# Kernel tuning notes

Hardware: AMD Instinct MI355X
Metric: run time of the kernel (lower is better)

The kernel has to match this reference:

```python
import jax, jax.numpy as jnp
import numpy as np

N_HEADS = 16
R = 256.0


def setup_inputs() -> dict:
    key = jax.random.key(0)
    ks = jax.random.split(key, 8)
    B, T, D, H = 4, 1024, 1024, N_HEADS
    s = 1.0 / np.sqrt(D)
    return {
        "x": jax.random.normal(ks[0], (B, T, D), jnp.float32),
        "Wq": jax.random.normal(ks[1], (D, D), jnp.float32) * s,
        "Wk": jax.random.normal(ks[2], (D, D), jnp.float32) * s,
        "Wv": jax.random.normal(ks[3], (D, D), jnp.float32) * s,
        "Wo": jax.random.normal(ks[4], (D, D), jnp.float32) * s,
        "bo": jnp.zeros((D,), jnp.float32),
        "Wspan": jax.random.normal(ks[5], (H, D), jnp.float32) * s,
        "bspan": jnp.zeros((H,), jnp.float32),
    }


def reference(x, Wq, Wk, Wv, Wo, bo, Wspan, bspan):
    B, T, D = x.shape
    H = N_HEADS
    dh = D // H
    scale = jnp.sqrt(jnp.float32(dh))

    # projections -> (B, H, T, dh)
    def proj(W):
        return jnp.einsum('btd,ed->bte', x, W).reshape(B, T, H, dh).transpose(0, 2, 1, 3)
    Q, K, V = proj(Wq), proj(Wk), proj(Wv)

    # learned span per head: z = T * sigmoid(span_net(mean_t x))  -> (B, H)
    z = T * jax.nn.sigmoid(jnp.einsum('bd,hd->bh', x.mean(axis=1), Wspan) + bspan)

    idx = jnp.arange(T, dtype=jnp.float32)
    dist = idx[None, :] - idx[:, None]          # dist[i,j] = j - i
    causal = dist >= 0                           # matches torch code's mask
    dist_c = jnp.maximum(dist, 0.0)

    scores = jnp.einsum('bhtd,bhsd->bhts', Q, K) / scale
    scores = jnp.where(causal[None, None], scores, -jnp.inf)
    attn = jax.nn.softmax(scores, axis=-1)

    # soft span mask chi_z(h) = clamp((R + z - dist)/R, 0, 1)  (Eq 7)
    span_mask = jnp.clip((R + z[:, :, None, None] - dist_c[None, None]) / R, 0.0, 1.0)
    attn = attn * span_mask
    attn = attn / (attn.sum(axis=-1, keepdims=True) + 1e-8)
    # dropout p=0.0 (eval) -> identity

    out = jnp.einsum('bhts,bhsd->bhtd', attn, V)
    out = out.transpose(0, 2, 1, 3).reshape(B, T, D)
    return jnp.einsum('btd,ed->bte', out, Wo) + bo
```

## Files before the change

kernel.cpp:

```cpp
#include <hip/hip_runtime.h>

#define T_SEQ 1024
#define D_MODEL 1024
#define NH 16
#define DH 64
#define R_SPAN 256.0f

typedef unsigned short ushort_t;
typedef __attribute__((ext_vector_type(8))) short bf16x8;
typedef __attribute__((ext_vector_type(4))) float f32x4;

__device__ __forceinline__ ushort_t f2bf(float f){
  union { float f; unsigned u; } v; v.f = f;
  unsigned r = v.u + 0x7fffu + ((v.u >> 16) & 1u);
  return (ushort_t)(r >> 16);
}

__device__ __forceinline__ ushort_t f2bf_fast(float f){
  union { float f; unsigned u; } v; v.f = f;
  return (ushort_t)((v.u + 0x8000u) >> 16);
}

__device__ __forceinline__ float fast_exp2(float x){
#if __has_builtin(__builtin_amdgcn_exp2f)
  return __builtin_amdgcn_exp2f(x);
#else
  return __expf(x * 0.69314718056f);
#endif
}

__device__ __forceinline__ void barrier_lds_only(){
  __builtin_amdgcn_s_waitcnt(0xC07F);
  __builtin_amdgcn_s_barrier();
}

typedef __attribute__((address_space(1))) void GV;
typedef __attribute__((address_space(3))) void LV;
__device__ __forceinline__ void gld16(const void* g, void* l){
  __builtin_amdgcn_global_load_lds((GV*)g, (LV*)l, 16, 0, 0);
}

__global__ void conv_w(const float* s1, const float* s2, const float* s3, const float* s4,
                       ushort_t* __restrict__ w_bf){
  const int chunk = blockIdx.y;
  const float* ws_[4] = {s1, s2, s3, s4};
  const float* src = ws_[chunk];
  ushort_t* dst = w_bf + ((size_t)chunk << 20);
  const int i = (blockIdx.x * 256 + threadIdx.x) * 4;
  float4 v = *(const float4*)(src + i);
  ushort4 o; o.x = f2bf(v.x); o.y = f2bf(v.y); o.z = f2bf(v.z); o.w = f2bf(v.w);
  *(ushort4*)(dst + i) = o;
}

__global__ void conv_mean_x(const float* __restrict__ x, ushort_t* __restrict__ x_bf,
                            float* __restrict__ pt){
  const int dc = blockIdx.x;
  const int b  = blockIdx.y;
  const int tc = blockIdx.z;
  const int tid = threadIdx.x;
  const int dl = tid & 63, tg = tid >> 6;
  const int d = dc * 256 + dl * 4;
  const size_t rowbase = ((size_t)b * T_SEQ + tc * 64 + tg * 16) * D_MODEL + d;
  const float* px = x + rowbase;
  ushort_t* pb = x_bf + rowbase;

  float s0 = 0.f, s1 = 0.f, s2 = 0.f, s3 = 0.f;
#pragma unroll
  for (int tt = 0; tt < 16; ++tt){
    float4 v = *(const float4*)(px + (size_t)tt * D_MODEL);
    ushort4 o; o.x = f2bf(v.x); o.y = f2bf(v.y); o.z = f2bf(v.z); o.w = f2bf(v.w);
    *(ushort4*)(pb + (size_t)tt * D_MODEL) = o;
    s0 += v.x; s1 += v.y; s2 += v.z; s3 += v.w;
  }

  __shared__ float red[4][256];
  *(float4*)&red[tg][dl * 4] = make_float4(s0, s1, s2, s3);
  __syncthreads();
  if (tg == 0){
    float4 a = *(float4*)&red[0][dl * 4];
    float4 c = *(float4*)&red[1][dl * 4];
    float4 e = *(float4*)&red[2][dl * 4];
    float4 g = *(float4*)&red[3][dl * 4];
    float4 t;
    t.x = a.x + c.x + e.x + g.x;
    t.y = a.y + c.y + e.y + g.y;
    t.z = a.z + c.z + e.z + g.z;
    t.w = a.w + c.w + e.w + g.w;
    *(float4*)&pt[((size_t)(tc * 4 + b) << 10) + d] = t;
  }
}

__global__ void span_kernel(const float* __restrict__ pt, const float* __restrict__ Wspan,
                            const float* __restrict__ bspan, float* __restrict__ z){
  const int h = blockIdx.x, b = blockIdx.y, tid = threadIdx.x;
  const float* wv = Wspan + h * D_MODEL;
  float s = 0.f;
  for (int i = tid; i < D_MODEL; i += 256){
    float acc = 0.f;
#pragma unroll
    for (int tc = 0; tc < 16; ++tc) acc += pt[((size_t)(tc * 4 + b) << 10) + i];
    s += acc * wv[i];
  }
  for (int off = 32; off; off >>= 1) s += __shfl_down(s, off, 64);
  __shared__ float r4[4];
  if ((tid & 63) == 0) r4[tid >> 6] = s;
  __syncthreads();
  if (tid == 0){
    float tot = r4[0] + r4[1] + r4[2] + r4[3];
    float logit = tot * (1.0f / T_SEQ) + bspan[h];
    z[b * NH + h] = (float)T_SEQ / (1.0f + __expf(-logit));
  }
}

template<int FP32OUT>
__global__ __launch_bounds__(512) void gemm_bt(
    const ushort_t* __restrict__ A,
    const ushort_t* __restrict__ B,
    void* __restrict__ C,
    const float* __restrict__ bias,
    const int M, const int N, const int K)
{
  __shared__ ushort_t At[2][128 * 32];
  __shared__ ushort_t Bt[2][128 * 32];

  const int z = blockIdx.z;
  const ushort_t* Bz = B + (size_t)z * N * K;

  const int tid = threadIdx.x;
  const int w = tid >> 6, lane = tid & 63;
  const int q = lane >> 4, c = lane & 15;
  const int m0 = blockIdx.y * 128, n0 = blockIdx.x * 128;
  const int wm = (w >> 2) * 64, wn = (w & 3) * 32;

  const int lr = lane >> 2;
  const int lc = (lane & 3) * 8;

  f32x4 acc[4][2] = {};

  const ushort_t* ga0 = A  + (size_t)(m0 + w * 16 + lr) * K + lc;
  const ushort_t* gb0 = Bz + (size_t)(n0 + w * 16 + lr) * K + lc;

  const int S = K >> 5;
  gld16(ga0, &At[0][(w * 16) * 32]);
  gld16(gb0, &Bt[0][(w * 16) * 32]);

  for (int s = 0; s < S; ++s){
    __syncthreads();
    if (s + 1 < S){
      const int k0 = (s + 1) << 5;
      const int nb = (s + 1) & 1;
      gld16(ga0 + k0, &At[nb][(w * 16) * 32]);
      gld16(gb0 + k0, &Bt[nb][(w * 16) * 32]);
    }
    const ushort_t* at = At[s & 1];
    const ushort_t* bt = Bt[s & 1];

    bf16x8 af[4], bfv[2];
#pragma unroll
    for (int i = 0; i < 4; ++i) af[i]  = *(const bf16x8*)&at[(wm + i * 16 + c) * 32 + q * 8];
#pragma unroll
    for (int j = 0; j < 2; ++j) bfv[j] = *(const bf16x8*)&bt[(wn + j * 16 + c) * 32 + q * 8];
#pragma unroll
    for (int i = 0; i < 4; ++i)
#pragma unroll
      for (int j = 0; j < 2; ++j)
        acc[i][j] = __builtin_amdgcn_mfma_f32_16x16x32_bf16(af[i], bfv[j], acc[i][j], 0, 0, 0);
  }

  if (FP32OUT){
#pragma unroll
    for (int i = 0; i < 4; ++i){
#pragma unroll
      for (int j = 0; j < 2; ++j){
        const int row = m0 + wm + i * 16 + q * 4;
        const int col = n0 + wn + j * 16 + c;
#pragma unroll
        for (int r = 0; r < 4; ++r)
          ((float*)C)[(size_t)(row + r) * N + col] = acc[i][j][r] + bias[col];
      }
    }
  } else if (z == 2){
    ushort_t* Cv = (ushort_t*)C + (size_t)2 * M * N;
    const int bb = m0 >> 10;
#pragma unroll
    for (int i = 0; i < 4; ++i){
#pragma unroll
      for (int j = 0; j < 2; ++j){
        const int col = n0 + wn + j * 16 + c;
        const int t0 = (m0 & 1023) + wm + i * 16 + q * 4;
        ushort4 pk;
        pk.x = f2bf_fast(acc[i][j][0]); pk.y = f2bf_fast(acc[i][j][1]);
        pk.z = f2bf_fast(acc[i][j][2]); pk.w = f2bf_fast(acc[i][j][3]);
        *(ushort4*)&Cv[((size_t)bb << 20) + (size_t)col * 1024 + t0] = pk;
      }
    }
  } else {
#pragma unroll
    for (int i = 0; i < 4; ++i){
#pragma unroll
      for (int j = 0; j < 2; ++j){
        const int row = m0 + wm + i * 16 + q * 4;
        const int col = n0 + wn + j * 16 + c;
#pragma unroll
        for (int r = 0; r < 4; ++r)
          ((ushort_t*)C + (size_t)z * M * N)[(size_t)(row + r) * N + col] = f2bf_fast(acc[i][j][r]);
      }
    }
  }
}

#define LP 72
__global__ __launch_bounds__(512) void attn_kernel(
    const ushort_t* __restrict__ Qg,
    const ushort_t* __restrict__ Kg,
    const ushort_t* __restrict__ Vtg,
    const float* __restrict__ zspan,
    ushort_t* __restrict__ Og)
{
  __shared__ ushort_t Qs[128 * LP];
  __shared__ ushort_t Ks[2][64 * LP];
  __shared__ ushort_t Vt[2][64 * LP];
  __shared__ ushort_t Ps[8][16 * LP];

  const int id = blockIdx.x;
  const int qt = (id >> 3) & 7;
  const int g  = ((id >> 6) << 3) | (id & 7);
  const int b = g >> 4, h = g & 15;
  const int q0 = qt * 128;
  const int tid = threadIdx.x, w = tid >> 6, lane = tid & 63;
  const int q = lane >> 4, c = lane & 15;

  const size_t base = ((size_t)b * T_SEQ) * D_MODEL + (size_t)h * DH;
  const ushort_t* vtb = Vtg + ((size_t)b << 20) + ((size_t)h << 16);

  {
    const int row = tid >> 2, seg = tid & 3;
    const uint4* gq = (const uint4*)(Qg + base + (size_t)(q0 + row) * D_MODEL);
    uint4* qs = (uint4*)&Qs[row * LP];
    qs[seg * 2]     = gq[seg * 2];
    qs[seg * 2 + 1] = gq[seg * 2 + 1];
  }

  const float zz = zspan[b * NH + h];
  const int jend = min(T_SEQ, (int)(q0 + 127 + R_SPAN + zz) + 1);

  f32x4 acc_d = {};
  f32x4 o[4] = {};

  bf16x8 ones8;
#pragma unroll
  for (int i = 0; i < 8; ++i) ones8[i] = (short)0x3F80;

  const int wi0 = q0 + w * 16, wi1 = wi0 + 15;
  int i_row[4];
  float ar4[4];
#pragma unroll
  for (int r = 0; r < 4; ++r){
    i_row[r] = wi0 + q * 4 + r;
    ar4[r] = (R_SPAN + zz + (float)i_row[r]) * (1.0f / R_SPAN);
  }
  float cjR[4];
#pragma unroll
  for (int jf = 0; jf < 4; ++jf) cjR[jf] = (float)(jf * 16 + c) * (1.0f / R_SPAN);
  const float kexp = 0.125f * 1.44269504f;

  const int srow = tid >> 3, sseg = tid & 7;
  const ushort_t* kg = Kg + base + sseg * 8;
  const ushort_t* vg = vtb + (size_t)srow * 1024 + sseg * 8;

  uint4 kreg = *(const uint4*)(kg + (size_t)(q0 + srow) * D_MODEL);
  uint4 vreg = *(const uint4*)(vg + q0);

  __syncthreads();
  const bf16x8 aq0 = *(const bf16x8*)&Qs[(w * 16 + c) * LP + q * 8];
  const bf16x8 aq1 = *(const bf16x8*)&Qs[(w * 16 + c) * LP + 32 + q * 8];

  int it = 0;
  for (int j0 = q0; j0 < jend; j0 += 64, ++it){
    const int buf = it & 1;
    *(uint4*)&Ks[buf][srow * LP + sseg * 8] = kreg;
    *(uint4*)&Vt[buf][srow * LP + sseg * 8] = vreg;
    if (j0 + 64 < jend){
      kreg = *(const uint4*)(kg + (size_t)(j0 + 64 + srow) * D_MODEL);
      vreg = *(const uint4*)(vg + j0 + 64);
    }
    barrier_lds_only();

    if (j0 + 63 < wi0) continue;
    if ((float)(j0 - wi1) > R_SPAN + zz) continue;

    f32x4 s[4] = {};
#pragma unroll
    for (int jf = 0; jf < 4; ++jf){
      bf16x8 bk0 = *(const bf16x8*)&Ks[buf][(jf * 16 + c) * LP + q * 8];
      s[jf] = __builtin_amdgcn_mfma_f32_16x16x32_bf16(aq0, bk0, s[jf], 0, 0, 0);
      bf16x8 bk1 = *(const bf16x8*)&Ks[buf][(jf * 16 + c) * LP + 32 + q * 8];
      s[jf] = __builtin_amdgcn_mfma_f32_16x16x32_bf16(aq1, bk1, s[jf], 0, 0, 0);
    }

    const bool need_mask = (j0 <= wi1);
    const bool full = ((float)(j0 + 63 - wi0) <= zz);

    if (full){
      if (need_mask){
#pragma unroll
        for (int jf = 0; jf < 4; ++jf){
          const int j = j0 + jf * 16 + c;
#pragma unroll
          for (int r = 0; r < 4; ++r){
            float p = fast_exp2(s[jf][r] * kexp);
            p = (j >= i_row[r]) ? p : 0.f;
            Ps[w][(q * 4 + r) * LP + jf * 16 + c] = f2bf_fast(p);
          }
        }
      } else {
#pragma unroll
        for (int jf = 0; jf < 4; ++jf){
#pragma unroll
          for (int r = 0; r < 4; ++r){
            float p = fast_exp2(s[jf][r] * kexp);
            Ps[w][(q * 4 + r) * LP + jf * 16 + c] = f2bf_fast(p);
          }
        }
      }
    } else {
      const float arj = (float)j0 * (1.0f / R_SPAN);
      if (need_mask){
#pragma unroll
        for (int jf = 0; jf < 4; ++jf){
          const int j = j0 + jf * 16 + c;
#pragma unroll
          for (int r = 0; r < 4; ++r){
            float p = fast_exp2(s[jf][r] * kexp);
            p = (j >= i_row[r]) ? p : 0.f;
            float chi = fminf(fmaxf((ar4[r] - arj) - cjR[jf], 0.f), 1.f);
            Ps[w][(q * 4 + r) * LP + jf * 16 + c] = f2bf_fast(p * chi);
          }
        }
      } else {
#pragma unroll
        for (int jf = 0; jf < 4; ++jf){
#pragma unroll
          for (int r = 0; r < 4; ++r){
            float p = fast_exp2(s[jf][r] * kexp);
            float chi = fminf(fmaxf((ar4[r] - arj) - cjR[jf], 0.f), 1.f);
            Ps[w][(q * 4 + r) * LP + jf * 16 + c] = f2bf_fast(p * chi);
          }
        }
      }
    }

    {
      bf16x8 pa0 = *(const bf16x8*)&Ps[w][c * LP + q * 8];
      bf16x8 pa1 = *(const bf16x8*)&Ps[w][c * LP + 32 + q * 8];
      acc_d = __builtin_amdgcn_mfma_f32_16x16x32_bf16(pa0, ones8, acc_d, 0, 0, 0);
      acc_d = __builtin_amdgcn_mfma_f32_16x16x32_bf16(pa1, ones8, acc_d, 0, 0, 0);
#pragma unroll
      for (int nf = 0; nf < 4; ++nf){
        bf16x8 bv0 = *(const bf16x8*)&Vt[buf][(nf * 16 + c) * LP + q * 8];
        o[nf] = __builtin_amdgcn_mfma_f32_16x16x32_bf16(pa0, bv0, o[nf], 0, 0, 0);
        bf16x8 bv1 = *(const bf16x8*)&Vt[buf][(nf * 16 + c) * LP + 32 + q * 8];
        o[nf] = __builtin_amdgcn_mfma_f32_16x16x32_bf16(pa1, bv1, o[nf], 0, 0, 0);
      }
    }
  }

#pragma unroll
  for (int r = 0; r < 4; ++r){
    const float inv = 1.0f / (acc_d[r] + 1e-20f);
    const size_t rowbase = base + (size_t)i_row[r] * D_MODEL;
#pragma unroll
    for (int nf = 0; nf < 4; ++nf){
      Og[rowbase + nf * 16 + c] = f2bf_fast(o[nf][r] * inv);
    }
  }
}

extern "C" void kernel_launch(void* const* d_in, const int* in_sizes, int n_in,
                              void* d_out, int out_size, void* d_ws, size_t ws_size,
                              hipStream_t stream)
{
  const float* x     = (const float*)d_in[0];
  const float* Wq    = (const float*)d_in[1];
  const float* Wk    = (const float*)d_in[2];
  const float* Wv    = (const float*)d_in[3];
  const float* Wo    = (const float*)d_in[4];
  const float* bo    = (const float*)d_in[5];
  const float* Wspan = (const float*)d_in[6];
  const float* bspan = (const float*)d_in[7];

  const size_t MT = (size_t)4 * T_SEQ;

  ushort_t* x_bf = (ushort_t*)d_ws;
  ushort_t* w_bf = x_bf + MT * D_MODEL;
  ushort_t* qkv  = w_bf + (size_t)4 * D_MODEL * D_MODEL;
  ushort_t* attn = qkv + (size_t)3 * MT * D_MODEL;
  float* pt      = (float*)(attn + MT * D_MODEL);
  float* zsp     = pt + 16 * 4 * D_MODEL;

  conv_w<<<dim3(1024, 4), 256, 0, stream>>>(Wq, Wk, Wv, Wo, w_bf);
  conv_mean_x<<<dim3(4, 4, 16), 256, 0, stream>>>(x, x_bf, pt);
  span_kernel<<<dim3(16, 4), 256, 0, stream>>>(pt, Wspan, bspan, zsp);

  gemm_bt<0><<<dim3(8, 32, 3), 512, 0, stream>>>(x_bf, w_bf, qkv, nullptr, 4096, 1024, 1024);

  attn_kernel<<<dim3(512), 512, 0, stream>>>(qkv, qkv + MT * D_MODEL,
                                             qkv + 2 * MT * D_MODEL, zsp, attn);

  gemm_bt<1><<<dim3(8, 32, 1), 512, 0, stream>>>(attn, w_bf + (size_t)3 * D_MODEL * D_MODEL,
                                                 d_out, bo, 4096, 1024, 1024);
}
```

Baseline: 179.4 us.

## Merge weight and input conversion kernels; reverse attention tile order for balance

Folds the weight bf16 conversion and the x conversion/mean kernels into a single prep launch, with each weight block now converting 16 float4 chunks per thread. This removes one kernel launch and its tail. Separately, the attention kernel reverses the query-tile order for the second half of the grid so heavy and light causal tiles are interleaved across the dispatch, which should even out per-CU work. The merged prep grid has fewer, larger blocks for the weight part, which may lower memory-level parallelism slightly.

Measured after the change: 171.1 us. 4.6% less time.

```diff
diff --git a/kernel.cpp b/kernel.cpp
--- a/kernel.cpp
+++ b/kernel.cpp
@@ -40,41 +40,50 @@
   __builtin_amdgcn_global_load_lds((GV*)g, (LV*)l, 16, 0, 0);
 }
 
-__global__ void conv_w(const float* s1, const float* s2, const float* s3, const float* s4,
-                       ushort_t* __restrict__ w_bf){
-  const int chunk = blockIdx.y;
-  const float* ws_[4] = {s1, s2, s3, s4};
-  const float* src = ws_[chunk];
-  ushort_t* dst = w_bf + ((size_t)chunk << 20);
-  const int i = (blockIdx.x * 256 + threadIdx.x) * 4;
-  float4 v = *(const float4*)(src + i);
-  ushort4 o; o.x = f2bf(v.x); o.y = f2bf(v.y); o.z = f2bf(v.z); o.w = f2bf(v.w);
-  *(ushort4*)(dst + i) = o;
-}
-
-__global__ void conv_mean_x(const float* __restrict__ x, ushort_t* __restrict__ x_bf,
+__global__ void prep_kernel(const float* __restrict__ x,
+                            const float* s1, const float* s2, const float* s3, const float* s4,
+                            ushort_t* __restrict__ x_bf, ushort_t* __restrict__ w_bf,
                             float* __restrict__ pt){
+  const int z = blockIdx.z;
+  const int tid = threadIdx.x;
+
+  if (z >= 16){
+    const int wz = z - 16;
+    const int chunk = wz >> 2;
+    const int sub = ((wz & 3) << 4) | (blockIdx.y << 2) | blockIdx.x;
+    const float* ws_[4] = {s1, s2, s3, s4};
+    const float* src = ws_[chunk] + (size_t)sub * 16384;
+    ushort_t* dst = w_bf + ((size_t)chunk << 20) + (size_t)sub * 16384;
+#pragma unroll
+    for (int i = 0; i < 16; ++i){
+      const int o = (i * 256 + tid) * 4;
+      float4 v = *(const float4*)(src + o);
+      ushort4 u; u.x = f2bf(v.x); u.y = f2bf(v.y); u.z = f2bf(v.z); u.w = f2bf(v.w);
+      *(ushort4*)(dst + o) = u;
+    }
+    return;
+  }
+
   const int dc = blockIdx.x;
   const int b  = blockIdx.y;
-  const int tc = blockIdx.z;
-  const int tid = threadIdx.x;
+  const int tc = z;
   const int dl = tid & 63, tg = tid >> 6;
   const int d = dc * 256 + dl * 4;
   const size_t rowbase = ((size_t)b * T_SEQ + tc * 64 + tg * 16) * D_MODEL + d;
   const float* px = x + rowbase;
   ushort_t* pb = x_bf + rowbase;
 
-  float s0 = 0.f, s1 = 0.f, s2 = 0.f, s3 = 0.f;
+  float s0 = 0.f, s1v = 0.f, s2v = 0.f, s3v = 0.f;
 #pragma unroll
   for (int tt = 0; tt < 16; ++tt){
     float4 v = *(const float4*)(px + (size_t)tt * D_MODEL);
     ushort4 o; o.x = f2bf(v.x); o.y = f2bf(v.y); o.z = f2bf(v.z); o.w = f2bf(v.w);
     *(ushort4*)(pb + (size_t)tt * D_MODEL) = o;
-    s0 += v.x; s1 += v.y; s2 += v.z; s3 += v.w;
+    s0 += v.x; s1v += v.y; s2v += v.z; s3v += v.w;
   }
 
   __shared__ float red[4][256];
-  *(float4*)&red[tg][dl * 4] = make_float4(s0, s1, s2, s3);
+  *(float4*)&red[tg][dl * 4] = make_float4(s0, s1v, s2v, s3v);
   __syncthreads();
   if (tg == 0){
     float4 a = *(float4*)&red[0][dl * 4];
@@ -223,7 +232,8 @@
   __shared__ ushort_t Ps[8][16 * LP];
 
   const int id = blockIdx.x;
-  const int qt = (id >> 3) & 7;
+  int qt = (id >> 3) & 7;
+  if (id >= 256) qt = 7 - qt;
   const int g  = ((id >> 6) << 3) | (id & 7);
   const int b = g >> 4, h = g & 15;
   const int q0 = qt * 128;
@@ -398,8 +408,7 @@
   float* pt      = (float*)(attn + MT * D_MODEL);
   float* zsp     = pt + 16 * 4 * D_MODEL;
 
-  conv_w<<<dim3(1024, 4), 256, 0, stream>>>(Wq, Wk, Wv, Wo, w_bf);
-  conv_mean_x<<<dim3(4, 4, 16), 256, 0, stream>>>(x, x_bf, pt);
+  prep_kernel<<<dim3(4, 4, 32), 256, 0, stream>>>(x, Wq, Wk, Wv, Wo, x_bf, w_bf, pt);
   span_kernel<<<dim3(16, 4), 256, 0, stream>>>(pt, Wspan, bspan, zsp);
 
   gemm_bt<0><<<dim3(8, 32, 3), 512, 0, stream>>>(x_bf, w_bf, qkv, nullptr, 4096, 1024, 1024);
```
